# Optimization experiments

Measured on AMD Instinct MI355X. Metric: run time of the kernel, lower is better.

## Reference

```python
import jax, jax.numpy as jnp
import numpy as np

L, B, E, H = 2048, 2, 1024, 16
D = E // H
R = E // 4  # self-space subspace rank
ALPHA = 0.6


def setup_inputs() -> dict:
    key = jax.random.key(0)
    ks = jax.random.split(key, 11)
    s = 0.02
    return {
        "x": jax.random.normal(ks[0], (L, B, E), jnp.float32),
        "attn_mask": jnp.zeros((L, L), jnp.float32),
        "Wq": jax.random.normal(ks[1], (E, E), jnp.float32) * s,
        "bq": jnp.zeros((E,), jnp.float32),
        "Wk": jax.random.normal(ks[2], (E, E), jnp.float32) * s,
        "bk": jnp.zeros((E,), jnp.float32),
        "Wv": jax.random.normal(ks[3], (E, E), jnp.float32) * s,
        "bv": jnp.zeros((E,), jnp.float32),
        "Wo": jax.random.normal(ks[4], (E, E), jnp.float32) * s,
        "bo": jnp.zeros((E,), jnp.float32),
        "U": jax.random.normal(ks[5], (E, R), jnp.float32) * (1.0 / np.sqrt(E)),
    }


def _condition(t, U):
    # self_space.condition: blend with projection onto learned subspace U
    # t: [..., E]
    return ALPHA * t + (1.0 - ALPHA) * ((t @ U) @ U.T)


def reference(x, attn_mask, Wq, bq, Wk, bk, Wv, bv, Wo, bo, U):
    # x: [L, B, E] (seq-first)
    Q = x @ Wq.T + bq
    K = x @ Wk.T + bk
    V = x @ Wv.T + bv
    Qc = _condition(Q, U)
    Kc = _condition(K, U)
    # split heads: [L, B, H, D]
    q = Qc.reshape(L, B, H, D)
    k = Kc.reshape(L, B, H, D)
    v = V.reshape(L, B, H, D)
    scores = jnp.einsum("lbhd,mbhd->bhlm", q, k) / jnp.sqrt(jnp.float32(D))
    scores = scores + attn_mask  # broadcast [L,L] over [B,H,L,L]
    attn_weights = jax.nn.softmax(scores, axis=-1)  # dropout p=0.0 -> identity
    ctx = jnp.einsum("bhlm,mbhd->lbhd", attn_weights, v).reshape(L, B, E)
    out = ctx @ Wo.T + bo
    return out, attn_weights  # attn_weights: [B, H, L, L]
```

## Files before the change

### kernel.cpp

```cpp
#include <hip/hip_runtime.h>
#include <cstddef>

#define L_SEQ  2048
#define B_SZ   2
#define E_DIM  1024
#define H_N    16
#define D_HEAD 64
#define R_DIM  256

typedef unsigned short u16;
using bf16x8 = __attribute__((ext_vector_type(8))) short;
using f32x4  = __attribute__((ext_vector_type(4))) float;

__device__ __forceinline__ u16 bf16rne(float f) {
    unsigned u = __float_as_uint(f);
    return (u16)((u + 0x7FFFu + ((u >> 16) & 1u)) >> 16);
}
__device__ __forceinline__ float b2f(u16 h) {
    return __uint_as_float(((unsigned)h) << 16);
}

__device__ __forceinline__ void gload16(const u16* g, u16* l) {
    __builtin_amdgcn_global_load_lds(
        (const __attribute__((address_space(1))) void*)g,
        (__attribute__((address_space(3))) void*)l, 16, 0, 0);
}

__global__ __launch_bounds__(256)
void convert_hilo(const float* __restrict__ in, u16* __restrict__ hi,
                  u16* __restrict__ lo, int n4)
{
    for (int i = blockIdx.x * 256 + threadIdx.x; i < n4; i += gridDim.x * 256) {
        float4 v = ((const float4*)in)[i];
        u16 h0 = bf16rne(v.x), h1 = bf16rne(v.y), h2 = bf16rne(v.z), h3 = bf16rne(v.w);
        uint2 hp;
        hp.x = (unsigned)h0 | ((unsigned)h1 << 16);
        hp.y = (unsigned)h2 | ((unsigned)h3 << 16);
        ((uint2*)hi)[i] = hp;
        u16 l0 = bf16rne(v.x - b2f(h0)), l1 = bf16rne(v.y - b2f(h1));
        u16 l2 = bf16rne(v.z - b2f(h2)), l3 = bf16rne(v.w - b2f(h3));
        uint2 lp;
        lp.x = (unsigned)l0 | ((unsigned)l1 << 16);
        lp.y = (unsigned)l2 | ((unsigned)l3 << 16);
        ((uint2*)lo)[i] = lp;
    }
}

__global__ __launch_bounds__(256)
void transpose_f32_hilo(const float* __restrict__ in, u16* __restrict__ oh,
                        u16* __restrict__ ol, int rows, int cols)
{
    __shared__ float t[32][33];
    const int tx = threadIdx.x & 31, ty = threadIdx.x >> 5;
    const int r0 = blockIdx.y * 32, c0 = blockIdx.x * 32;
    #pragma unroll
    for (int i = 0; i < 4; i++)
        t[ty + i * 8][tx] = in[(size_t)(r0 + ty + i * 8) * cols + c0 + tx];
    __syncthreads();
    #pragma unroll
    for (int i = 0; i < 4; i++) {
        float v = t[tx][ty + i * 8];
        u16 h = bf16rne(v);
        size_t o = (size_t)(c0 + ty + i * 8) * rows + r0 + tx;
        oh[o] = h;
        ol[o] = bf16rne(v - b2f(h));
    }
}

__global__ __launch_bounds__(256)
void transpose_v_bf16(const u16* __restrict__ vh, u16* __restrict__ vt)
{
    __shared__ u16 t[32][34];
    const int tx = threadIdx.x & 31, ty = threadIdx.x >> 5;
    const int l0 = blockIdx.x * 32, d0 = blockIdx.y * 32;
    const int z = blockIdx.z, b = z >> 4, h = z & 15;
    #pragma unroll
    for (int i = 0; i < 4; i++)
        t[ty + i * 8][tx] =
            vh[(size_t)((l0 + ty + i * 8) * B_SZ + b) * E_DIM + h * D_HEAD + d0 + tx];
    __syncthreads();
    #pragma unroll
    for (int i = 0; i < 4; i++)
        vt[(size_t)(z * D_HEAD + d0 + ty + i * 8) * L_SEQ + l0 + tx] = t[tx][ty + i * 8];
}

__global__ void flag_init(int* f) { if (threadIdx.x == 0) *f = 0; }

__global__ __launch_bounds__(256)
void mask_scan(const float* __restrict__ m, int* __restrict__ f, int n4)
{
    int nz = 0;
    for (int i = blockIdx.x * 256 + threadIdx.x; i < n4; i += gridDim.x * 256) {
        float4 v = ((const float4*)m)[i];
        nz |= (v.x != 0.0f) | (v.y != 0.0f) | (v.z != 0.0f) | (v.w != 0.0f);
    }
    if (nz) atomicOr(f, 1);
}

__global__ __launch_bounds__(256)
void bias_fold1(const float* __restrict__ b, const float* __restrict__ U,
                float* __restrict__ tmp)
{
    const int r = threadIdx.x;
    float s = 0.0f;
    for (int e = 0; e < E_DIM; e++) s += U[(size_t)e * R_DIM + r] * b[e];
    tmp[r] = s;
}

__global__ __launch_bounds__(256)
void bias_fold2(const float* __restrict__ b, const float* __restrict__ U,
                const float* __restrict__ tmp, float* __restrict__ beff)
{
    const int e = blockIdx.x * 256 + threadIdx.x;
    float s = 0.0f;
    for (int r = 0; r < R_DIM; r++) s += U[(size_t)e * R_DIM + r] * tmp[r];
    beff[e] = 0.6f * b[e] + 0.4f * s;
}

template <bool SPLIT>
__global__ __launch_bounds__(256)
void gemm_mfma(const u16* __restrict__ Ah, const u16* __restrict__ Al,
               const u16* __restrict__ Bh, const u16* __restrict__ Bl,
               float* __restrict__ Cf, u16* __restrict__ Ch, u16* __restrict__ Cl,
               const u16* __restrict__ Cinh, const u16* __restrict__ Cinl,
               const float* __restrict__ bias,
               int M, int N, int K, int lda, int ldb, int ldc,
               float alpha, float beta)
{
    constexpr int BM = 128, BN = 128, BK = 64;
    constexpr int ALO = BM * BK, BLO = BN * BK;
    __shared__ __align__(16) u16 As[(SPLIT ? 2 : 1) * BM * BK];
    __shared__ __align__(16) u16 Bs[(SPLIT ? 2 : 1) * BN * BK];

    const int tid = threadIdx.x;
    const int tm = blockIdx.y * BM, tn = blockIdx.x * BN;
    const int lane = tid & 63;
    const int fr = lane & 15, kg = lane >> 4;
    const int wave = tid >> 6;
    const int wm = (wave >> 1) * 64, wn = (wave & 1) * 64;

    const int sR8 = lane >> 3;
    const int sG  = ((lane & 7) ^ sR8) * 8;

    f32x4 acc[4][4] = {};

    for (int k0 = 0; k0 < K; k0 += BK) {
        #pragma unroll
        for (int c = 0; c < 4; c++) {
            const int r0 = (c * 4 + wave) * 8;
            gload16(Ah + (size_t)(tm + r0 + sR8) * lda + k0 + sG, &As[r0 * BK]);
            gload16(Bh + (size_t)(tn + r0 + sR8) * ldb + k0 + sG, &Bs[r0 * BK]);
            if constexpr (SPLIT) {
                gload16(Al + (size_t)(tm + r0 + sR8) * lda + k0 + sG, &As[ALO + r0 * BK]);
                gload16(Bl + (size_t)(tn + r0 + sR8) * ldb + k0 + sG, &Bs[BLO + r0 * BK]);
            }
        }
        __syncthreads();

        #pragma unroll
        for (int ks = 0; ks < 2; ks++) {
            bf16x8 ah[4], al[4];
            #pragma unroll
            for (int m = 0; m < 4; m++) {
                int row = wm + m * 16 + fr;
                int p = (ks * 4 + kg) ^ (row & 7);
                ah[m] = *(const bf16x8*)&As[row * BK + p * 8];
                if constexpr (SPLIT)
                    al[m] = *(const bf16x8*)&As[ALO + row * BK + p * 8];
            }
            #pragma unroll
            for (int n = 0; n < 4; n++) {
                int col = wn + n * 16 + fr;
                int p = (ks * 4 + kg) ^ (col & 7);
                bf16x8 bh = *(const bf16x8*)&Bs[col * BK + p * 8];
                #pragma unroll
                for (int m = 0; m < 4; m++)
                    acc[m][n] = __builtin_amdgcn_mfma_f32_16x16x32_bf16(ah[m], bh, acc[m][n], 0, 0, 0);
                if constexpr (SPLIT) {
                    bf16x8 bl = *(const bf16x8*)&Bs[BLO + col * BK + p * 8];
                    #pragma unroll
                    for (int m = 0; m < 4; m++) {
                        acc[m][n] = __builtin_amdgcn_mfma_f32_16x16x32_bf16(al[m], bh, acc[m][n], 0, 0, 0);
                        acc[m][n] = __builtin_amdgcn_mfma_f32_16x16x32_bf16(ah[m], bl, acc[m][n], 0, 0, 0);
                    }
                }
            }
        }
        __syncthreads();
    }

    #pragma unroll
    for (int m = 0; m < 4; m++) {
        int row0 = tm + wm + m * 16 + kg * 4;
        #pragma unroll
        for (int n = 0; n < 4; n++) {
            int col = tn + wn + n * 16 + fr;
            float bv = bias ? bias[col] : 0.0f;
            #pragma unroll
            for (int j = 0; j < 4; j++) {
                size_t idx = (size_t)(row0 + j) * ldc + col;
                float v = alpha * acc[m][n][j] + bv;
                if (beta != 0.0f) {
                    float ci = b2f(Cinh[idx]);
                    if (Cinl) ci += b2f(Cinl[idx]);
                    v += beta * ci;
                }
                if (Cf) Cf[idx] = v;
                if (Ch) {
                    u16 h = bf16rne(v);
                    Ch[idx] = h;
                    if (Cl) Cl[idx] = bf16rne(v - b2f(h));
                }
            }
        }
    }
}

__global__ __launch_bounds__(256)
void attn_fused(const u16* __restrict__ Qc, const u16* __restrict__ Kc,
                const u16* __restrict__ Vt, float* __restrict__ attn,
                u16* __restrict__ ctxh, u16* __restrict__ ctxl,
                const float* __restrict__ mask, const int* __restrict__ maskFlag)
{
    __shared__ __align__(16) u16 Qs[64 * 64];
    __shared__ __align__(16) u16 Ks[64 * 64];
    __shared__ __align__(16) u16 Vs[64 * 64];
    __shared__ __align__(16) u16 Ps[4][16 * 64];

    const int tid = threadIdx.x;
    const int z  = blockIdx.y;
    const int q0 = blockIdx.x * 64;
    const int qkOff = (z >> 4) * E_DIM + (z & 15) * D_HEAD;
    const long vtOff = (long)z * D_HEAD * L_SEQ;
    const long aOff  = (long)z * L_SEQ * L_SEQ;
    const int ldq = B_SZ * E_DIM;

    const int lane = tid & 63;
    const int fr = lane & 15, kg = lane >> 4;
    const int wave = tid >> 6;
    const int wq = wave * 16;

    const bool useMask = maskFlag[0] != 0;
    const int sR8 = lane >> 3;
    const int sG  = ((lane & 7) ^ sR8) * 8;

    #pragma unroll
    for (int c = 0; c < 2; c++) {
        const int r0 = (c * 4 + wave) * 8;
        gload16(Qc + (size_t)(q0 + r0 + sR8) * ldq + qkOff + sG, &Qs[r0 * 64]);
    }
    __syncthreads();
    bf16x8 qf[2];
    #pragma unroll
    for (int ks = 0; ks < 2; ks++) {
        int row = wq + fr;
        qf[ks] = *(const bf16x8*)&Qs[row * 64 + ((ks * 4 + kg) ^ (row & 7)) * 8];
    }
    __syncthreads();

    float mrow[4], lrow[4];
    #pragma unroll
    for (int j = 0; j < 4; j++) { mrow[j] = -3.4e38f; lrow[j] = 0.0f; }

    for (int kt = 0; kt < L_SEQ / 64; kt++) {
        const int kv0 = kt * 64;
        #pragma unroll
        for (int c = 0; c < 2; c++) {
            const int r0 = (c * 4 + wave) * 8;
            gload16(Kc + (size_t)(kv0 + r0 + sR8) * ldq + qkOff + sG, &Ks[r0 * 64]);
        }
        __syncthreads();

        f32x4 acc[4] = {};
        #pragma unroll
        for (int ks = 0; ks < 2; ks++) {
            #pragma unroll
            for (int n = 0; n < 4; n++) {
                int col = n * 16 + fr;
                bf16x8 bh = *(const bf16x8*)&Ks[col * 64 + ((ks * 4 + kg) ^ (col & 7)) * 8];
                acc[n] = __builtin_amdgcn_mfma_f32_16x16x32_bf16(qf[ks], bh, acc[n], 0, 0, 0);
            }
        }
        __syncthreads();

        #pragma unroll
        for (int j = 0; j < 4; j++) {
            float v[4];
            #pragma unroll
            for (int n = 0; n < 4; n++) {
                v[n] = acc[n][j] * 0.125f;
                if (useMask)
                    v[n] += mask[(size_t)(q0 + wq + kg * 4 + j) * L_SEQ + kv0 + n * 16 + fr];
            }
            float t0 = fmaxf(fmaxf(v[0], v[1]), fmaxf(v[2], v[3]));
            float nm = fmaxf(mrow[j], t0);
            float sc = __expf(mrow[j] - nm);
            float s  = __expf(v[0] - nm) + __expf(v[1] - nm)
                     + __expf(v[2] - nm) + __expf(v[3] - nm);
            lrow[j] = lrow[j] * sc + s;
            mrow[j] = nm;
        }
    }

    #pragma unroll
    for (int j = 0; j < 4; j++) {
        float m_ = mrow[j], l_ = lrow[j];
        #pragma unroll
        for (int off = 1; off < 16; off <<= 1) {
            float mo = __shfl_xor(m_, off, 64);
            float lo2 = __shfl_xor(l_, off, 64);
            float M = fmaxf(m_, mo);
            l_ = l_ * __expf(m_ - M) + lo2 * __expf(mo - M);
            m_ = M;
        }
        mrow[j] = m_;
        lrow[j] = 1.0f / l_;
    }

    u16* Pw = &Ps[wave][0];
    f32x4 acc_o[4] = {};

    for (int kt = 0; kt < L_SEQ / 64; kt++) {
        const int kv0 = kt * 64;
        #pragma unroll
        for (int c = 0; c < 2; c++) {
            const int r0 = (c * 4 + wave) * 8;
            gload16(Kc + (size_t)(kv0 + r0 + sR8) * ldq + qkOff + sG, &Ks[r0 * 64]);
            gload16(Vt + vtOff + (size_t)(r0 + sR8) * L_SEQ + kv0 + sG, &Vs[r0 * 64]);
        }
        __syncthreads();

        f32x4 acc[4] = {};
        #pragma unroll
        for (int ks = 0; ks < 2; ks++) {
            #pragma unroll
            for (int n = 0; n < 4; n++) {
                int col = n * 16 + fr;
                bf16x8 bh = *(const bf16x8*)&Ks[col * 64 + ((ks * 4 + kg) ^ (col & 7)) * 8];
                acc[n] = __builtin_amdgcn_mfma_f32_16x16x32_bf16(qf[ks], bh, acc[n], 0, 0, 0);
            }
        }

        #pragma unroll
        for (int n = 0; n < 4; n++) {
            #pragma unroll
            for (int j = 0; j < 4; j++) {
                int row = kg * 4 + j;
                int col = n * 16 + fr;
                float v = acc[n][j] * 0.125f;
                if (useMask)
                    v += mask[(size_t)(q0 + wq + row) * L_SEQ + kv0 + col];
                float p = __expf(v - mrow[j]) * lrow[j];
                attn[aOff + (size_t)(q0 + wq + row) * L_SEQ + kv0 + col] = p;
                Pw[row * 64 + ((col >> 3) ^ (row & 7)) * 8 + (col & 7)] = bf16rne(p);
            }
        }

        asm volatile("" ::: "memory");

        #pragma unroll
        for (int ks = 0; ks < 2; ks++) {
            int rowA = fr;
            bf16x8 pa = *(const bf16x8*)&Pw[rowA * 64 + ((ks * 4 + kg) ^ (rowA & 7)) * 8];
            #pragma unroll
            for (int n = 0; n < 4; n++) {
                int d = n * 16 + fr;
                bf16x8 vb = *(const bf16x8*)&Vs[d * 64 + ((ks * 4 + kg) ^ (d & 7)) * 8];
                acc_o[n] = __builtin_amdgcn_mfma_f32_16x16x32_bf16(pa, vb, acc_o[n], 0, 0, 0);
            }
        }
        __syncthreads();
    }

    #pragma unroll
    for (int n = 0; n < 4; n++) {
        #pragma unroll
        for (int j = 0; j < 4; j++) {
            int row = q0 + wq + kg * 4 + j;
            int d = n * 16 + fr;
            float v = acc_o[n][j];
            size_t idx = (size_t)row * ldq + qkOff + d;
            u16 h = bf16rne(v);
            ctxh[idx] = h;
            ctxl[idx] = bf16rne(v - b2f(h));
        }
    }
}

extern "C" void kernel_launch(void* const* d_in, const int* in_sizes, int n_in,
                              void* d_out, int out_size, void* d_ws, size_t ws_size,
                              hipStream_t stream)
{
    const float* x    = (const float*)d_in[0];
    const float* mask = (const float*)d_in[1];
    const float* Wq   = (const float*)d_in[2];
    const float* bq   = (const float*)d_in[3];
    const float* Wk   = (const float*)d_in[4];
    const float* bk   = (const float*)d_in[5];
    const float* Wv   = (const float*)d_in[6];
    const float* bv   = (const float*)d_in[7];
    const float* Wo   = (const float*)d_in[8];
    const float* bo   = (const float*)d_in[9];
    const float* U    = (const float*)d_in[10];

    float* out   = (float*)d_out;
    float* attnF = out + (size_t)L_SEQ * B_SZ * E_DIM;

    const int SZ  = L_SEQ * B_SZ * E_DIM;
    const int WSZ = E_DIM * E_DIM;
    const int USZ = E_DIM * R_DIM;

    u16* Qch  = (u16*)d_ws;
    u16* Kch  = Qch + SZ;
    u16* Vth  = Kch + SZ;
    u16* ctxh = Vth + SZ;
    u16* ctxl = ctxh + SZ;
    u16* Woh  = ctxl + SZ;
    u16* Wol  = Woh + WSZ;
    int* maskFlag = (int*)(Wol + WSZ);

    u16* sc   = (u16*)attnF;
    u16* xh   = sc;          u16* xl   = xh + SZ;
    u16* Wqh  = xl + SZ;     u16* Wql  = Wqh + WSZ;
    u16* Wkh  = Wql + WSZ;   u16* Wkl  = Wkh + WSZ;
    u16* Wvh  = Wkl + WSZ;   u16* Wvl  = Wvh + WSZ;
    u16* Uh   = Wvl + WSZ;   u16* Ul   = Uh + USZ;
    u16* Uth  = Ul + USZ;    u16* Utl  = Uth + USZ;
    u16* WqTh = Utl + USZ;   u16* WqTl = WqTh + WSZ;
    u16* WkTh = WqTl + WSZ;  u16* WkTl = WkTh + WSZ;
    u16* GTqh = WkTl + WSZ;  u16* GTql = GTqh + USZ;
    u16* GTkh = GTql + USZ;  u16* GTkl = GTkh + USZ;
    u16* Wfqh = GTkl + USZ;  u16* Wfql = Wfqh + WSZ;
    u16* Wfkh = Wfql + WSZ;  u16* Wfkl = Wfkh + WSZ;
    u16* Vh   = Wfkl + WSZ;
    float* bqe  = (float*)(Vh + SZ);
    float* bke  = bqe + E_DIM;
    float* tmpv = bke + E_DIM;

    const dim3 blk(256);
    const int M = L_SEQ * B_SZ;

    hipLaunchKernelGGL(flag_init, dim3(1), dim3(64), 0, stream, maskFlag);
    hipLaunchKernelGGL(mask_scan, dim3(512), blk, 0, stream,
                       mask, maskFlag, (L_SEQ * L_SEQ) / 4);

    hipLaunchKernelGGL(convert_hilo, dim3(2048), blk, 0, stream, x,  xh,  xl,  SZ / 4);
    hipLaunchKernelGGL(convert_hilo, dim3(512),  blk, 0, stream, Wq, Wqh, Wql, WSZ / 4);
    hipLaunchKernelGGL(convert_hilo, dim3(512),  blk, 0, stream, Wk, Wkh, Wkl, WSZ / 4);
    hipLaunchKernelGGL(convert_hilo, dim3(512),  blk, 0, stream, Wv, Wvh, Wvl, WSZ / 4);
    hipLaunchKernelGGL(convert_hilo, dim3(512),  blk, 0, stream, Wo, Woh, Wol, WSZ / 4);
    hipLaunchKernelGGL(convert_hilo, dim3(128),  blk, 0, stream, U,  Uh,  Ul,  USZ / 4);
    hipLaunchKernelGGL(transpose_f32_hilo, dim3(R_DIM / 32, E_DIM / 32), blk, 0, stream,
                       U, Uth, Utl, E_DIM, R_DIM);
    hipLaunchKernelGGL(transpose_f32_hilo, dim3(E_DIM / 32, E_DIM / 32), blk, 0, stream,
                       Wq, WqTh, WqTl, E_DIM, E_DIM);
    hipLaunchKernelGGL(transpose_f32_hilo, dim3(E_DIM / 32, E_DIM / 32), blk, 0, stream,
                       Wk, WkTh, WkTl, E_DIM, E_DIM);

    hipLaunchKernelGGL(bias_fold1, dim3(1), blk, 0, stream, bq, U, tmpv);
    hipLaunchKernelGGL(bias_fold2, dim3(E_DIM / 256), blk, 0, stream, bq, U, tmpv, bqe);
    hipLaunchKernelGGL(bias_fold1, dim3(1), blk, 0, stream, bk, U, tmpv);
    hipLaunchKernelGGL(bias_fold2, dim3(E_DIM / 256), blk, 0, stream, bk, U, tmpv, bke);

    {
        dim3 gt(R_DIM / 128, E_DIM / 128, 1);
        dim3 gw(E_DIM / 128, E_DIM / 128, 1);
        hipLaunchKernelGGL((gemm_mfma<true>), gt, blk, 0, stream,
            WqTh, WqTl, Uth, Utl, nullptr, GTqh, GTql, nullptr, nullptr, nullptr,
            E_DIM, R_DIM, E_DIM, E_DIM, E_DIM, R_DIM, 1.0f, 0.0f);
        hipLaunchKernelGGL((gemm_mfma<true>), gw, blk, 0, stream,
            Uh, Ul, GTqh, GTql, nullptr, Wfqh, Wfql, Wqh, Wql, nullptr,
            E_DIM, E_DIM, R_DIM, R_DIM, R_DIM, E_DIM, 0.4f, 0.6f);
        hipLaunchKernelGGL((gemm_mfma<true>), gt, blk, 0, stream,
            WkTh, WkTl, Uth, Utl, nullptr, GTkh, GTkl, nullptr, nullptr, nullptr,
            E_DIM, R_DIM, E_DIM, E_DIM, E_DIM, R_DIM, 1.0f, 0.0f);
        hipLaunchKernelGGL((gemm_mfma<true>), gw, blk, 0, stream,
            Uh, Ul, GTkh, GTkl, nullptr, Wfkh, Wfkl, Wkh, Wkl, nullptr,
            E_DIM, E_DIM, R_DIM, R_DIM, R_DIM, E_DIM, 0.4f, 0.6f);
    }

    {
        dim3 g(E_DIM / 128, M / 128, 1);
        hipLaunchKernelGGL((gemm_mfma<true>), g, blk, 0, stream,
            xh, xl, Wfqh, Wfql, nullptr, Qch, nullptr, nullptr, nullptr, bqe,
            M, E_DIM, E_DIM, E_DIM, E_DIM, E_DIM, 1.0f, 0.0f);
        hipLaunchKernelGGL((gemm_mfma<true>), g, blk, 0, stream,
            xh, xl, Wfkh, Wfkl, nullptr, Kch, nullptr, nullptr, nullptr, bke,
            M, E_DIM, E_DIM, E_DIM, E_DIM, E_DIM, 1.0f, 0.0f);
        hipLaunchKernelGGL((gemm_mfma<true>), g, blk, 0, stream,
            xh, xl, Wvh, Wvl, nullptr, Vh, nullptr, nullptr, nullptr, bv,
            M, E_DIM, E_DIM, E_DIM, E_DIM, E_DIM, 1.0f, 0.0f);
    }
    hipLaunchKernelGGL(transpose_v_bf16, dim3(L_SEQ / 32, D_HEAD / 32, B_SZ * H_N),
                       blk, 0, stream, Vh, Vth);

    hipLaunchKernelGGL(attn_fused, dim3(L_SEQ / 64, B_SZ * H_N), blk, 0, stream,
                       Qch, Kch, Vth, attnF, ctxh, ctxl, mask, maskFlag);

    {
        dim3 g(E_DIM / 128, M / 128, 1);
        hipLaunchKernelGGL((gemm_mfma<true>), g, blk, 0, stream,
            ctxh, ctxl, Woh, Wol, out, nullptr, nullptr, nullptr, nullptr, bo,
            M, E_DIM, E_DIM, E_DIM, E_DIM, E_DIM, 1.0f, 0.0f);
    }
}
```

Before: 1.151 ms.

## Batch projection GEMMs via grid z-dimension and template tile sizes

Makes the MFMA GEMM templated on block tile size and adds per-z strides. The separate Q/K weight-fold GEMMs and the Q/K/V projection GEMMs are each merged into single batched launches, with workspace buffers reordered so the batched operands sit at fixed strides. Smaller tiles (64x64 and 128x64) raise the block count so more of the CUs are busy and fewer kernels are launched. The cost is less data reuse per tile and a mask flag now stored in the last element of the output buffer, which the final GEMM overwrites later.

```diff
diff --git a/kernel.cpp b/kernel.cpp
--- a/kernel.cpp
+++ b/kernel.cpp
@@ -98,6 +98,13 @@
 }
 
 __global__ __launch_bounds__(256)
+void copy_f32(const float* __restrict__ s, float* __restrict__ d, int n)
+{
+    int i = blockIdx.x * 256 + threadIdx.x;
+    if (i < n) d[i] = s[i];
+}
+
+__global__ __launch_bounds__(256)
 void bias_fold1(const float* __restrict__ b, const float* __restrict__ U,
                 float* __restrict__ tmp)
 {
@@ -117,7 +124,7 @@
     beff[e] = 0.6f * b[e] + 0.4f * s;
 }
 
-template <bool SPLIT>
+template <int BM, int BN, bool SPLIT>
 __global__ __launch_bounds__(256)
 void gemm_mfma(const u16* __restrict__ Ah, const u16* __restrict__ Al,
                const u16* __restrict__ Bh, const u16* __restrict__ Bl,
@@ -125,43 +132,52 @@
                const u16* __restrict__ Cinh, const u16* __restrict__ Cinl,
                const float* __restrict__ bias,
                int M, int N, int K, int lda, int ldb, int ldc,
+               long aStr, long bStr, long cStr, long biasStr,
                float alpha, float beta)
 {
-    constexpr int BM = 128, BN = 128, BK = 64;
+    constexpr int BK = 64;
+    constexpr int FM = BM / 32, FN = BN / 32;
     constexpr int ALO = BM * BK, BLO = BN * BK;
     __shared__ __align__(16) u16 As[(SPLIT ? 2 : 1) * BM * BK];
     __shared__ __align__(16) u16 Bs[(SPLIT ? 2 : 1) * BN * BK];
 
     const int tid = threadIdx.x;
+    const int z = blockIdx.z;
+    const long aOff = z * aStr, bOff = z * bStr, cOff = z * cStr;
+    const long biasOff = z * biasStr;
     const int tm = blockIdx.y * BM, tn = blockIdx.x * BN;
     const int lane = tid & 63;
     const int fr = lane & 15, kg = lane >> 4;
     const int wave = tid >> 6;
-    const int wm = (wave >> 1) * 64, wn = (wave & 1) * 64;
+    const int wm = (wave >> 1) * (BM / 2), wn = (wave & 1) * (BN / 2);
 
     const int sR8 = lane >> 3;
     const int sG  = ((lane & 7) ^ sR8) * 8;
 
-    f32x4 acc[4][4] = {};
+    f32x4 acc[FM][FN] = {};
 
     for (int k0 = 0; k0 < K; k0 += BK) {
         #pragma unroll
-        for (int c = 0; c < 4; c++) {
+        for (int c = 0; c < BM / 32; c++) {
             const int r0 = (c * 4 + wave) * 8;
-            gload16(Ah + (size_t)(tm + r0 + sR8) * lda + k0 + sG, &As[r0 * BK]);
-            gload16(Bh + (size_t)(tn + r0 + sR8) * ldb + k0 + sG, &Bs[r0 * BK]);
-            if constexpr (SPLIT) {
-                gload16(Al + (size_t)(tm + r0 + sR8) * lda + k0 + sG, &As[ALO + r0 * BK]);
-                gload16(Bl + (size_t)(tn + r0 + sR8) * ldb + k0 + sG, &Bs[BLO + r0 * BK]);
-            }
+            gload16(Ah + aOff + (size_t)(tm + r0 + sR8) * lda + k0 + sG, &As[r0 * BK]);
+            if constexpr (SPLIT)
+                gload16(Al + aOff + (size_t)(tm + r0 + sR8) * lda + k0 + sG, &As[ALO + r0 * BK]);
+        }
+        #pragma unroll
+        for (int c = 0; c < BN / 32; c++) {
+            const int r0 = (c * 4 + wave) * 8;
+            gload16(Bh + bOff + (size_t)(tn + r0 + sR8) * ldb + k0 + sG, &Bs[r0 * BK]);
+            if constexpr (SPLIT)
+                gload16(Bl + bOff + (size_t)(tn + r0 + sR8) * ldb + k0 + sG, &Bs[BLO + r0 * BK]);
         }
         __syncthreads();
 
         #pragma unroll
         for (int ks = 0; ks < 2; ks++) {
-            bf16x8 ah[4], al[4];
-            #pragma unroll
-            for (int m = 0; m < 4; m++) {
+            bf16x8 ah[FM], al[FM];
+            #pragma unroll
+            for (int m = 0; m < FM; m++) {
                 int row = wm + m * 16 + fr;
                 int p = (ks * 4 + kg) ^ (row & 7);
                 ah[m] = *(const bf16x8*)&As[row * BK + p * 8];
@@ -169,17 +185,17 @@
                     al[m] = *(const bf16x8*)&As[ALO + row * BK + p * 8];
             }
             #pragma unroll
-            for (int n = 0; n < 4; n++) {
+            for (int n = 0; n < FN; n++) {
                 int col = wn + n * 16 + fr;
                 int p = (ks * 4 + kg) ^ (col & 7);
                 bf16x8 bh = *(const bf16x8*)&Bs[col * BK + p * 8];
                 #pragma unroll
-                for (int m = 0; m < 4; m++)
+                for (int m = 0; m < FM; m++)
                     acc[m][n] = __builtin_amdgcn_mfma_f32_16x16x32_bf16(ah[m], bh, acc[m][n], 0, 0, 0);
                 if constexpr (SPLIT) {
                     bf16x8 bl = *(const bf16x8*)&Bs[BLO + col * BK + p * 8];
                     #pragma unroll
-                    for (int m = 0; m < 4; m++) {
+                    for (int m = 0; m < FM; m++) {
                         acc[m][n] = __builtin_amdgcn_mfma_f32_16x16x32_bf16(al[m], bh, acc[m][n], 0, 0, 0);
                         acc[m][n] = __builtin_amdgcn_mfma_f32_16x16x32_bf16(ah[m], bl, acc[m][n], 0, 0, 0);
                     }
@@ -190,15 +206,15 @@
     }
 
     #pragma unroll
-    for (int m = 0; m < 4; m++) {
+    for (int m = 0; m < FM; m++) {
         int row0 = tm + wm + m * 16 + kg * 4;
         #pragma unroll
-        for (int n = 0; n < 4; n++) {
+        for (int n = 0; n < FN; n++) {
             int col = tn + wn + n * 16 + fr;
-            float bv = bias ? bias[col] : 0.0f;
+            float bv = bias ? bias[biasOff + col] : 0.0f;
             #pragma unroll
             for (int j = 0; j < 4; j++) {
-                size_t idx = (size_t)(row0 + j) * ldc + col;
+                size_t idx = cOff + (size_t)(row0 + j) * ldc + col;
                 float v = alpha * acc[m][n][j] + bv;
                 if (beta != 0.0f) {
                     float ci = b2f(Cinh[idx]);
@@ -412,30 +428,29 @@
 
     u16* Qch  = (u16*)d_ws;
     u16* Kch  = Qch + SZ;
-    u16* Vth  = Kch + SZ;
+    u16* Vh   = Kch + SZ;
+    u16* Vth  = Vh + SZ;
     u16* ctxh = Vth + SZ;
     u16* ctxl = ctxh + SZ;
     u16* Woh  = ctxl + SZ;
     u16* Wol  = Woh + WSZ;
-    int* maskFlag = (int*)(Wol + WSZ);
+    int* maskFlag = (int*)(out + (size_t)SZ) - 1;
 
     u16* sc   = (u16*)attnF;
     u16* xh   = sc;          u16* xl   = xh + SZ;
     u16* Wqh  = xl + SZ;     u16* Wql  = Wqh + WSZ;
     u16* Wkh  = Wql + WSZ;   u16* Wkl  = Wkh + WSZ;
-    u16* Wvh  = Wkl + WSZ;   u16* Wvl  = Wvh + WSZ;
+    u16* Wfqh = Wkl + WSZ;   u16* Wfql = Wfqh + WSZ;
+    u16* Wfkh = Wfql + WSZ;  u16* Wfkl = Wfkh + WSZ;
+    u16* Wvh  = Wfkl + WSZ;  u16* Wvl  = Wvh + WSZ;
     u16* Uh   = Wvl + WSZ;   u16* Ul   = Uh + USZ;
     u16* Uth  = Ul + USZ;    u16* Utl  = Uth + USZ;
     u16* WqTh = Utl + USZ;   u16* WqTl = WqTh + WSZ;
     u16* WkTh = WqTl + WSZ;  u16* WkTl = WkTh + WSZ;
     u16* GTqh = WkTl + WSZ;  u16* GTql = GTqh + USZ;
     u16* GTkh = GTql + USZ;  u16* GTkl = GTkh + USZ;
-    u16* Wfqh = GTkl + USZ;  u16* Wfql = Wfqh + WSZ;
-    u16* Wfkh = Wfql + WSZ;  u16* Wfkl = Wfkh + WSZ;
-    u16* Vh   = Wfkl + WSZ;
-    float* bqe  = (float*)(Vh + SZ);
-    float* bke  = bqe + E_DIM;
-    float* tmpv = bke + E_DIM;
+    float* bqkv = (float*)(GTkl + USZ);
+    float* tmpv = bqkv + 3 * E_DIM;
 
     const dim3 blk(256);
     const int M = L_SEQ * B_SZ;
@@ -458,49 +473,33 @@
                        Wk, WkTh, WkTl, E_DIM, E_DIM);
 
     hipLaunchKernelGGL(bias_fold1, dim3(1), blk, 0, stream, bq, U, tmpv);
-    hipLaunchKernelGGL(bias_fold2, dim3(E_DIM / 256), blk, 0, stream, bq, U, tmpv, bqe);
+    hipLaunchKernelGGL(bias_fold2, dim3(E_DIM / 256), blk, 0, stream, bq, U, tmpv, bqkv);
     hipLaunchKernelGGL(bias_fold1, dim3(1), blk, 0, stream, bk, U, tmpv);
-    hipLaunchKernelGGL(bias_fold2, dim3(E_DIM / 256), blk, 0, stream, bk, U, tmpv, bke);
-
-    {
-        dim3 gt(R_DIM / 128, E_DIM / 128, 1);
-        dim3 gw(E_DIM / 128, E_DIM / 128, 1);
-        hipLaunchKernelGGL((gemm_mfma<true>), gt, blk, 0, stream,
-            WqTh, WqTl, Uth, Utl, nullptr, GTqh, GTql, nullptr, nullptr, nullptr,
-            E_DIM, R_DIM, E_DIM, E_DIM, E_DIM, R_DIM, 1.0f, 0.0f);
-        hipLaunchKernelGGL((gemm_mfma<true>), gw, blk, 0, stream,
-            Uh, Ul, GTqh, GTql, nullptr, Wfqh, Wfql, Wqh, Wql, nullptr,
-            E_DIM, E_DIM, R_DIM, R_DIM, R_DIM, E_DIM, 0.4f, 0.6f);
-        hipLaunchKernelGGL((gemm_mfma<true>), gt, blk, 0, stream,
-            WkTh, WkTl, Uth, Utl, nullptr, GTkh, GTkl, nullptr, nullptr, nullptr,
-            E_DIM, R_DIM, E_DIM, E_DIM, E_DIM, R_DIM, 1.0f, 0.0f);
-        hipLaunchKernelGGL((gemm_mfma<true>), gw, blk, 0, stream,
-            Uh, Ul, GTkh, GTkl, nullptr, Wfkh, Wfkl, Wkh, Wkl, nullptr,
-            E_DIM, E_DIM, R_DIM, R_DIM, R_DIM, E_DIM, 0.4f, 0.6f);
-    }
-
-    {
-        dim3 g(E_DIM / 128, M / 128, 1);
-        hipLaunchKernelGGL((gemm_mfma<true>), g, blk, 0, stream,
-            xh, xl, Wfqh, Wfql, nullptr, Qch, nullptr, nullptr, nullptr, bqe,
-            M, E_DIM, E_DIM, E_DIM, E_DIM, E_DIM, 1.0f, 0.0f);
-        hipLaunchKernelGGL((gemm_mfma<true>), g, blk, 0, stream,
-            xh, xl, Wfkh, Wfkl, nullptr, Kch, nullptr, nullptr, nullptr, bke,
-            M, E_DIM, E_DIM, E_DIM, E_DIM, E_DIM, 1.0f, 0.0f);
-        hipLaunchKernelGGL((gemm_mfma<true>), g, blk, 0, stream,
-            xh, xl, Wvh, Wvl, nullptr, Vh, nullptr, nullptr, nullptr, bv,
-            M, E_DIM, E_DIM, E_DIM, E_DIM, E_DIM, 1.0f, 0.0f);
-    }
+    hipLaunchKernelGGL(bias_fold2, dim3(E_DIM / 256), blk, 0, stream, bk, U, tmpv, bqkv + E_DIM);
+    hipLaunchKernelGGL(copy_f32, dim3(E_DIM / 256), blk, 0, stream, bv, bqkv + 2 * E_DIM, E_DIM);
+
+    hipLaunchKernelGGL((gemm_mfma<64, 64, true>), dim3(R_DIM / 64, E_DIM / 64, 2), blk, 0, stream,
+        WqTh, WqTl, Uth, Utl, nullptr, GTqh, GTqh + USZ, nullptr, nullptr, nullptr,
+        E_DIM, R_DIM, E_DIM, E_DIM, E_DIM, R_DIM,
+        (long)2 * WSZ, 0L, (long)2 * USZ, 0L, 1.0f, 0.0f);
+    hipLaunchKernelGGL((gemm_mfma<64, 64, true>), dim3(E_DIM / 64, E_DIM / 64, 2), blk, 0, stream,
+        Uh, Ul, GTqh, GTqh + USZ, nullptr, Wfqh, Wfqh + WSZ, Wqh, Wqh + WSZ, nullptr,
+        E_DIM, E_DIM, R_DIM, R_DIM, R_DIM, E_DIM,
+        0L, (long)2 * USZ, (long)2 * WSZ, 0L, 0.4f, 0.6f);
+
+    hipLaunchKernelGGL((gemm_mfma<128, 64, true>), dim3(E_DIM / 64, M / 128, 3), blk, 0, stream,
+        xh, xl, Wfqh, Wfqh + WSZ, nullptr, Qch, nullptr, nullptr, nullptr, bqkv,
+        M, E_DIM, E_DIM, E_DIM, E_DIM, E_DIM,
+        0L, (long)2 * WSZ, (long)SZ, (long)E_DIM, 1.0f, 0.0f);
+
     hipLaunchKernelGGL(transpose_v_bf16, dim3(L_SEQ / 32, D_HEAD / 32, B_SZ * H_N),
                        blk, 0, stream, Vh, Vth);
 
     hipLaunchKernelGGL(attn_fused, dim3(L_SEQ / 64, B_SZ * H_N), blk, 0, stream,
                        Qch, Kch, Vth, attnF, ctxh, ctxl, mask, maskFlag);
 
-    {
-        dim3 g(E_DIM / 128, M / 128, 1);
-        hipLaunchKernelGGL((gemm_mfma<true>), g, blk, 0, stream,
-            ctxh, ctxl, Woh, Wol, out, nullptr, nullptr, nullptr, nullptr, bo,
-            M, E_DIM, E_DIM, E_DIM, E_DIM, E_DIM, 1.0f, 0.0f);
-    }
-}
+    hipLaunchKernelGGL((gemm_mfma<128, 64, true>), dim3(E_DIM / 64, M / 128, 1), blk, 0, stream,
+        ctxh, ctxl, Woh, Wol, out, nullptr, nullptr, nullptr, nullptr, bo,
+        M, E_DIM, E_DIM, E_DIM, E_DIM, E_DIM,
+        0L, 0L, 0L, 0L, 1.0f, 0.0f);
+}
```

Result: faster. 1.007 ms (-12.5%).
